# Performance work log

Measured on AMD Instinct MI355X. Metric: run time of the kernel, lower is better.

Reference implementation:

```python
import jax, jax.numpy as jnp
import numpy as np

HIDDEN = 2560
NUM_HEADS = 80
HEAD_DIM = 64
STATE = 128
N_GROUPS = 1
CONV_K = 4
CHUNK = 256
INTER = 2 * HIDDEN                       # 5120 = NUM_HEADS * HEAD_DIM
CONV_DIM = INTER + 2 * N_GROUPS * STATE  # 5376
PROJ = INTER + CONV_DIM + NUM_HEADS      # 10576
EPS = 1e-5
DT_MIN, DT_MAX = 0.0, 100.0


def segment_sum(x):
    # x: (..., T) -> (..., T, T); out[i, j] = sum_{j < k <= i} x[k], -inf above diag
    T = x.shape[-1]
    xe = jnp.broadcast_to(x[..., :, None], x.shape + (T,))  # [i, j] = x[i]
    mask_lo = jnp.tril(jnp.ones((T, T), dtype=bool), -1)
    seg = jnp.cumsum(jnp.where(mask_lo, xe, 0.0), axis=-2)
    mask = jnp.tril(jnp.ones((T, T), dtype=bool), 0)
    return jnp.where(mask, seg, -jnp.inf)


def setup_inputs() -> dict:
    key = jax.random.key(0)
    k0, k1, k2, k3 = jax.random.split(key, 4)
    x = jax.random.normal(k0, (2, 2048, HIDDEN), jnp.float32)
    in_proj_w = jax.random.normal(k1, (PROJ, HIDDEN), jnp.float32) * (HIDDEN ** -0.5)
    conv1d_w = jax.random.normal(k2, (CONV_DIM, CONV_K), jnp.float32) * (CONV_K ** -0.5)
    conv1d_b = jnp.zeros((CONV_DIM,), jnp.float32)
    A_log = jnp.log(jnp.arange(1, NUM_HEADS + 1, dtype=jnp.float32))
    D = jnp.ones((NUM_HEADS,), jnp.float32)
    dt_bias = jnp.ones((NUM_HEADS,), jnp.float32)
    norm_weight = jnp.ones((INTER,), jnp.float32)
    out_proj_w = jax.random.normal(k3, (HIDDEN, INTER), jnp.float32) * (INTER ** -0.5)
    return dict(input_states=x, in_proj_w=in_proj_w, conv1d_w=conv1d_w,
                conv1d_b=conv1d_b, A_log=A_log, D=D, dt_bias=dt_bias,
                norm_weight=norm_weight, out_proj_w=out_proj_w)


def _mamba2_forward(input_states, in_proj_w, conv1d_w, conv1d_b, A_log, D,
                    dt_bias, norm_weight, out_proj_w):
    b, s, _ = input_states.shape
    proj = input_states @ in_proj_w.T                       # (b, s, PROJ)
    gate, hs, dt = jnp.split(proj, [INTER, INTER + CONV_DIM], axis=-1)

    # causal depthwise conv1d + SiLU
    xT = jnp.transpose(hs, (0, 2, 1))                       # (b, conv_dim, s)
    xT = jnp.pad(xT, ((0, 0), (0, 0), (CONV_K - 1, 0)))
    conv = jax.lax.conv_general_dilated(
        xT, conv1d_w[:, None, :], (1,), 'VALID',
        feature_group_count=CONV_DIM, dimension_numbers=('NCH', 'OIH', 'NCH'))
    hs = jax.nn.silu(jnp.transpose(conv + conv1d_b[None, :, None], (0, 2, 1)))

    hs, B, C = jnp.split(hs, [INTER, INTER + N_GROUPS * STATE], axis=-1)
    A = -jnp.exp(A_log)                                     # (h,)
    dt = jnp.clip(jax.nn.softplus(dt + dt_bias), DT_MIN, DT_MAX)  # (b, s, h)

    X = hs.reshape(b, s, NUM_HEADS, HEAD_DIM)
    rep = NUM_HEADS // N_GROUPS
    B = jnp.repeat(B.reshape(b, s, N_GROUPS, STATE), rep, axis=2)
    C = jnp.repeat(C.reshape(b, s, N_GROUPS, STATE), rep, axis=2)

    pad = (-s) % CHUNK
    D_res = D[None, None, :, None] * jnp.pad(X, ((0, 0), (0, pad), (0, 0), (0, 0)))
    Xd = X * dt[..., None]                                  # discretized input
    dA = A[None, None, :] * dt                              # (b, s, h)

    def chunk(t):
        t = jnp.pad(t, [(0, 0), (0, pad)] + [(0, 0)] * (t.ndim - 2))
        return t.reshape(t.shape[0], -1, CHUNK, *t.shape[2:])

    Xc, Bc, Cc = chunk(Xd), chunk(B), chunk(C)              # (b, c, l, h, ...)
    Ac = jnp.transpose(chunk(dA), (0, 3, 1, 2))             # (b, h, c, l)
    A_cum = jnp.cumsum(Ac, axis=-1)

    # 1. intra-chunk (diagonal block) outputs
    L = jnp.exp(segment_sum(Ac))                            # (b, h, c, l, l)
    G = jnp.einsum('bclhn,bcshn->bhcls', Cc, Bc)
    Y_diag = jnp.einsum('bhcls,bcshp->bclhp', G * L, Xc)

    # 2. per-chunk final states
    decay_states = jnp.exp(A_cum[..., -1:] - A_cum)         # (b, h, c, l)
    states = jnp.einsum('bclhn,bhcl,bclhp->bchpn', Bc, decay_states, Xc)

    # 3. inter-chunk recurrence
    A_last = A_cum[..., -1]                                 # (b, h, c)
    decay_chunk = jnp.exp(segment_sum(jnp.pad(A_last, ((0, 0), (0, 0), (1, 0)))))
    states = jnp.concatenate([jnp.zeros_like(states[:, :1]), states], axis=1)
    new_states = jnp.einsum('bhzc,bchpn->bzhpn', decay_chunk, states)
    states = new_states[:, :-1]                             # (b, c, h, p, n)

    # 4. state -> output conversion
    Y_off = jnp.einsum('bclhn,bchpn,bhcl->bclhp', Cc, states, jnp.exp(A_cum))

    y = (Y_diag + Y_off).reshape(b, -1, NUM_HEADS, HEAD_DIM) + D_res
    y = y[:, :s].reshape(b, s, INTER)

    # gated RMSNorm
    y = y * jax.nn.silu(gate)
    var = jnp.mean(y * y, axis=-1, keepdims=True)
    y = y * jax.lax.rsqrt(var + EPS) * norm_weight
    return y @ out_proj_w.T


def reference(input_states, in_proj_w, conv1d_w, conv1d_b, A_log, D, dt_bias,
              norm_weight, out_proj_w):
    return _mamba2_forward(input_states, in_proj_w, conv1d_w, conv1d_b, A_log,
                           D, dt_bias, norm_weight, out_proj_w)
```

## Files before the change

kernel.cpp:

```cpp
#include <hip/hip_runtime.h>
#include <hip/hip_bf16.h>
#include <math.h>

#define HIDDEN   2560
#define NUM_HEADS 80
#define HEAD_DIM 64
#define STATE    128
#define CONV_K   4
#define CHUNK    256
#define INTER    (2*HIDDEN)
#define CONV_DIM (INTER + 2*STATE)
#define PROJ     (INTER + CONV_DIM + NUM_HEADS)
#define PROJ_PAD 10624
#define NBC      336
#define NBCP     384
#define EPS      1e-5f

#define BATCH 2
#define SEQ   2048
#define TOK   (BATCH*SEQ)
#define NC    (SEQ/CHUNK)
#define KSPL2 8
#define KCH2  (HIDDEN/KSPL2)

typedef __attribute__((ext_vector_type(8))) short bf16x8;
typedef __attribute__((ext_vector_type(4))) float f32x4;

#define MFMA16(a,b,c) __builtin_amdgcn_mfma_f32_16x16x32_bf16((a),(b),(c),0,0,0)

__device__ __forceinline__ unsigned short f2bf(float f){
    union{float f;unsigned u;}v; v.f=f;
    unsigned r = v.u + 0x7fffu + ((v.u>>16)&1u);
    return (unsigned short)(r>>16);
}
__device__ __forceinline__ float bf2f(unsigned short s){
    union{unsigned u;float f;}v; v.u = ((unsigned)s)<<16; return v.f;
}
__device__ __forceinline__ void unpack8(uint4 u, float* e){
    e[0]=bf2f((unsigned short)(u.x&0xffff)); e[1]=bf2f((unsigned short)(u.x>>16));
    e[2]=bf2f((unsigned short)(u.y&0xffff)); e[3]=bf2f((unsigned short)(u.y>>16));
    e[4]=bf2f((unsigned short)(u.z&0xffff)); e[5]=bf2f((unsigned short)(u.z>>16));
    e[6]=bf2f((unsigned short)(u.w&0xffff)); e[7]=bf2f((unsigned short)(u.w>>16));
}

__device__ __forceinline__ void gld16(const void* g, void* l){
    __builtin_amdgcn_global_load_lds((const __attribute__((address_space(1))) void*)g,
                                     (__attribute__((address_space(3))) void*)l, 16, 0, 0);
}

template<bool BF16OUT>
__global__ __launch_bounds__(256) void gemm_bf16(const unsigned short* __restrict__ A, int lda,
                                                 const unsigned short* __restrict__ B, int ldb,
                                                 void* __restrict__ Cv, int ldc, int K) {
    __shared__ unsigned short As[128][64];
    __shared__ unsigned short Bs[128][64];
    int tid = threadIdx.x;
    int lane = tid & 63, wid = tid >> 6;
    int wr = wid >> 1, wc = wid & 1;

    int bm, bn;
    if ((gridDim.y & 7) == 0) {
        int bid   = blockIdx.y * gridDim.x + blockIdx.x;
        int xcd   = bid & 7;
        int local = bid >> 3;
        int mrows = gridDim.y >> 3;
        bm = (xcd * mrows + (local % mrows)) * 128;
        bn = (local / mrows) * 128;
    } else {
        bm = blockIdx.y * 128;
        bn = blockIdx.x * 128;
    }

    f32x4 acc[4][4];
    #pragma unroll
    for (int i=0;i<4;i++)
        #pragma unroll
        for (int j=0;j<4;j++) acc[i][j] = (f32x4){0.f,0.f,0.f,0.f};

    int srow_off = lane >> 3;
    int sslot    = lane & 7;

    for (int k0 = 0; k0 < K; k0 += 64) {
        #pragma unroll
        for (int q=0;q<4;q++){
            int brow = (wid*4+q)*8;
            int row  = brow + srow_off;
            int sl   = sslot ^ (row & 7);
            gld16(A + (size_t)(bm + row)*lda + k0 + sl*8, &As[brow][0]);
            gld16(B + (size_t)(bn + row)*ldb + k0 + sl*8, &Bs[brow][0]);
        }
        __syncthreads();
        #pragma unroll
        for (int kk=0; kk<64; kk+=32){
            bf16x8 a[4], b[4];
            #pragma unroll
            for (int i=0;i<4;i++){
                int row = wr*64 + i*16 + (lane&15);
                int slot = ((kk>>3) + (lane>>4)) ^ (row & 7);
                a[i] = *(const bf16x8*)&As[row][slot*8];
            }
            #pragma unroll
            for (int j=0;j<4;j++){
                int row = wc*64 + j*16 + (lane&15);
                int slot = ((kk>>3) + (lane>>4)) ^ (row & 7);
                b[j] = *(const bf16x8*)&Bs[row][slot*8];
            }
            #pragma unroll
            for (int i=0;i<4;i++)
                #pragma unroll
                for (int j=0;j<4;j++)
                    acc[i][j] = MFMA16(a[i], b[j], acc[i][j]);
        }
        __syncthreads();
    }
    #pragma unroll
    for (int i=0;i<4;i++){
        int row0 = bm + wr*64 + i*16 + (lane>>4)*4;
        #pragma unroll
        for (int j=0;j<4;j++){
            int col = bn + wc*64 + j*16 + (lane&15);
            #pragma unroll
            for (int r=0;r<4;r++){
                if (BF16OUT)
                    ((unsigned short*)Cv)[(size_t)(row0+r)*ldc + col] = f2bf(acc[i][j][r]);
                else
                    ((float*)Cv)[(size_t)(row0+r)*ldc + col] = acc[i][j][r];
            }
        }
    }
}

__global__ __launch_bounds__(256) void bc_splitk_mfma(const unsigned short* __restrict__ xhi,
                                                      const unsigned short* __restrict__ xlo,
                                                      const unsigned short* __restrict__ whi,
                                                      const unsigned short* __restrict__ wlo,
                                                      float* __restrict__ Cpart) {
    __shared__ unsigned short As[128][64];
    __shared__ unsigned short Bs[128][64];
    int tid = threadIdx.x;
    int lane = tid & 63, wid = tid >> 6;
    int wr = wid >> 1, wc = wid & 1;
    int bn = blockIdx.x * 128, bm = blockIdx.y * 128, z = blockIdx.z;

    f32x4 acc[4][4];
    #pragma unroll
    for (int i=0;i<4;i++)
        #pragma unroll
        for (int j=0;j<4;j++) acc[i][j] = (f32x4){0.f,0.f,0.f,0.f};

    int srow_off = lane >> 3;
    int sslot    = lane & 7;

    for (int term = 0; term < 3; ++term){
        const unsigned short* A = (term==2) ? xlo : xhi;
        const unsigned short* B = (term==0) ? wlo : whi;
        for (int k0 = z*KCH2; k0 < z*KCH2 + KCH2; k0 += 64) {
            #pragma unroll
            for (int q=0;q<4;q++){
                int brow = (wid*4+q)*8;
                int row  = brow + srow_off;
                int sl   = sslot ^ (row & 7);
                gld16(A + (size_t)(bm + row)*HIDDEN + k0 + sl*8, &As[brow][0]);
                gld16(B + (size_t)(bn + row)*HIDDEN + k0 + sl*8, &Bs[brow][0]);
            }
            __syncthreads();
            #pragma unroll
            for (int kk=0; kk<64; kk+=32){
                bf16x8 a[4], b[4];
                #pragma unroll
                for (int i=0;i<4;i++){
                    int row = wr*64 + i*16 + (lane&15);
                    int slot = ((kk>>3) + (lane>>4)) ^ (row & 7);
                    a[i] = *(const bf16x8*)&As[row][slot*8];
                }
                #pragma unroll
                for (int j=0;j<4;j++){
                    int row = wc*64 + j*16 + (lane&15);
                    int slot = ((kk>>3) + (lane>>4)) ^ (row & 7);
                    b[j] = *(const bf16x8*)&Bs[row][slot*8];
                }
                #pragma unroll
                for (int i=0;i<4;i++)
                    #pragma unroll
                    for (int j=0;j<4;j++)
                        acc[i][j] = MFMA16(a[i], b[j], acc[i][j]);
            }
            __syncthreads();
        }
    }
    float* Cz = Cpart + (size_t)z*TOK*NBCP;
    #pragma unroll
    for (int i=0;i<4;i++){
        int row0 = bm + wr*64 + i*16 + (lane>>4)*4;
        #pragma unroll
        for (int j=0;j<4;j++){
            int col = bn + wc*64 + j*16 + (lane&15);
            #pragma unroll
            for (int r=0;r<4;r++)
                Cz[(size_t)(row0+r)*NBCP + col] = acc[i][j][r];
        }
    }
}

__global__ __launch_bounds__(256) void reduce_bc2(const float* __restrict__ part,
                                                  const float* __restrict__ dt_bias,
                                                  float* __restrict__ outBC,
                                                  float* __restrict__ dtbuf) {
    size_t i4 = (size_t)blockIdx.x*256 + threadIdx.x;
    if (i4 >= (size_t)TOK*NBCP/4) return;
    size_t i = i4*4;
    float4 s = *(const float4*)(part + i);
    #pragma unroll
    for (int z=1; z<KSPL2; z++){
        float4 v = *(const float4*)(part + (size_t)z*TOK*NBCP + i);
        s.x += v.x; s.y += v.y; s.z += v.z; s.w += v.w;
    }
    int col = (int)(i % NBCP);
    int t   = (int)(i / NBCP);
    if (col < 256) {
        *(float4*)(outBC + (size_t)t*NBC + col) = s;
    } else if (col < NBC) {
        int h = col - 256;
        float e[4] = {s.x, s.y, s.z, s.w};
        #pragma unroll
        for (int u=0;u<4;u++){
            float xv = e[u] + dt_bias[h+u];
            float sp = (xv > 20.f) ? xv : log1pf(expf(xv));
            e[u] = fminf(fmaxf(sp, 0.f), 100.f);
        }
        float4 o; o.x=e[0]; o.y=e[1]; o.z=e[2]; o.w=e[3];
        *(float4*)(dtbuf + (size_t)t*NUM_HEADS + h) = o;
    }
}

#define N4A ((size_t)TOK*HIDDEN/4)
#define N4B ((size_t)PROJ_PAD*HIDDEN/4)
#define N4C ((size_t)NBCP*HIDDEN/4)
__global__ __launch_bounds__(256) void prep_kernel(const float* __restrict__ x,
                                                   const float* __restrict__ in_w,
                                                   unsigned short* __restrict__ xhi,
                                                   unsigned short* __restrict__ xlo,
                                                   unsigned short* __restrict__ w1b,
                                                   unsigned short* __restrict__ wbc_hi,
                                                   unsigned short* __restrict__ wbc_lo) {
    size_t gid = (size_t)blockIdx.x*256 + threadIdx.x;
    if (gid < N4A) {
        size_t i = gid*4;
        float4 v = *(const float4*)(x + i);
        float e[4] = {v.x, v.y, v.z, v.w};
        ushort4 h, l;
        unsigned short* hp = (unsigned short*)&h;
        unsigned short* lp = (unsigned short*)&l;
        #pragma unroll
        for (int u=0;u<4;u++){
            unsigned short hv = f2bf(e[u]);
            hp[u] = hv;
            lp[u] = f2bf(e[u] - bf2f(hv));
        }
        *(ushort4*)(xhi + i) = h;
        *(ushort4*)(xlo + i) = l;
    } else if (gid < N4A + N4B) {
        size_t j = gid - N4A;
        size_t i = j*4;
        int row = (int)(i / HIDDEN);
        ushort4 o;
        if (row < PROJ){
            float4 v = *(const float4*)(in_w + i);
            o.x=f2bf(v.x); o.y=f2bf(v.y); o.z=f2bf(v.z); o.w=f2bf(v.w);
        } else { o.x=o.y=o.z=o.w=0; }
        *(ushort4*)(w1b + i) = o;
    } else {
        size_t j = gid - N4A - N4B;
        size_t i = j*4;
        int row = (int)(i / HIDDEN);
        int kk  = (int)(i % HIDDEN);
        ushort4 h, l;
        h.x=h.y=h.z=h.w=0; l.x=l.y=l.z=l.w=0;
        if (row < NBC){
            float4 v = *(const float4*)(in_w + (size_t)(2*INTER + row)*HIDDEN + kk);
            float e[4] = {v.x, v.y, v.z, v.w};
            unsigned short* hp = (unsigned short*)&h;
            unsigned short* lp = (unsigned short*)&l;
            #pragma unroll
            for (int u=0;u<4;u++){
                unsigned short hv = f2bf(e[u]);
                hp[u] = hv;
                lp[u] = f2bf(e[u] - bf2f(hv));
            }
        }
        *(ushort4*)(wbc_hi + i) = h;
        *(ushort4*)(wbc_lo + i) = l;
    }
}

__global__ __launch_bounds__(256) void cvt_bf16(const float* __restrict__ in,
                                                unsigned short* __restrict__ out, size_t n4){
    size_t i4 = (size_t)blockIdx.x*256 + threadIdx.x;
    if (i4 >= n4) return;
    size_t i = i4*4;
    float4 v = *(const float4*)(in+i);
    ushort4 o; o.x=f2bf(v.x); o.y=f2bf(v.y); o.z=f2bf(v.z); o.w=f2bf(v.w);
    *(ushort4*)(out+i) = o;
}

__global__ __launch_bounds__(256) void conv_fused(const unsigned short* __restrict__ projb,
                                                  const float* __restrict__ projBC,
                                                  const float* __restrict__ cw,
                                                  const float* __restrict__ cb,
                                                  unsigned short* __restrict__ XT,
                                                  float* __restrict__ xBC_BC,
                                                  unsigned short* __restrict__ BT) {
    __shared__ unsigned short raw[68][66];
    int bid = blockIdx.x;
    int tid = threadIdx.x;
    if (bid < (TOK/64)*(INTER/64)) {
        int bx = bid & 63, by = bid >> 6;
        int t0 = bx * 64, d0 = by * 64;
        int b  = t0 / SEQ;
        int s0 = t0 % SEQ;
        for (int f = tid; f < 67*8; f += 256){
            int r = f >> 3, g = f & 7;
            int sp = s0 - 3 + r;
            uint4 v;
            if (sp >= 0) v = *(const uint4*)(projb + ((size_t)(b*SEQ+sp))*PROJ_PAD + INTER + d0 + g*8);
            else { v.x=0u; v.y=0u; v.z=0u; v.w=0u; }
            unsigned int* dst = (unsigned int*)&raw[r][g*8];
            dst[0]=v.x; dst[1]=v.y; dst[2]=v.z; dst[3]=v.w;
        }
        __syncthreads();
        int t = tid & 63, dg = tid >> 6;
        #pragma unroll
        for (int dd = 0; dd < 16; dd++){
            int d = dg*16 + dd;
            float acc = cb[d0+d];
            #pragma unroll
            for (int j=0;j<CONV_K;j++)
                acc += cw[(d0+d)*CONV_K+j] * bf2f(raw[t+j][d]);
            float val = acc/(1.f+expf(-acc));
            XT[((size_t)(b*INTER + d0 + d))*SEQ + s0 + t] = f2bf(val);
        }
    } else {
        int idx = (bid - (TOK/64)*(INTER/64))*256 + tid;
        if (idx >= TOK*256) return;
        int d = idx & 255;
        int t = idx >> 8;
        int b = t / SEQ, sl = t % SEQ;
        int dc = INTER + d;
        float acc = cb[dc];
        #pragma unroll
        for (int j=0;j<CONV_K;j++){
            int sp = sl - (CONV_K-1) + j;
            if (sp >= 0)
                acc += cw[dc*CONV_K+j] * projBC[((size_t)(b*SEQ+sp))*NBC + d];
        }
        float val = acc / (1.f + expf(-acc));
        xBC_BC[(size_t)t*256 + d] = val;
        if (d < 128)
            BT[((size_t)(b*128 + d))*SEQ + sl] = f2bf(val);
    }
}

__global__ __launch_bounds__(256) void cumsum_kernel(const float* __restrict__ dtbuf,
                                                     const float* __restrict__ A_log,
                                                     float* __restrict__ A_cum) {
    int c = blockIdx.x, h = blockIdx.y, b = blockIdx.z;
    int l = threadIdx.x;
    float A = -expf(A_log[h]);
    float v = A * dtbuf[(size_t)(b*SEQ + c*CHUNK + l)*NUM_HEADS + h];
    __shared__ float buf[CHUNK];
    buf[l] = v;
    __syncthreads();
    for (int off=1; off<CHUNK; off<<=1){
        float t = (l>=off) ? buf[l-off] : 0.f;
        __syncthreads();
        buf[l] += t;
        __syncthreads();
    }
    A_cum[((size_t)b*NUM_HEADS + h)*SEQ + c*CHUNK + l] = buf[l];
}

__global__ __launch_bounds__(256) void g_kernel(const float* __restrict__ xBC_BC,
                                                unsigned short* __restrict__ G) {
    int p = blockIdx.x, c = blockIdx.y, b = blockIdx.z;
    int lt = 0, a0 = 0;
    while (a0 + lt + 1 <= p) { a0 += lt + 1; lt++; }
    int st = p - a0;
    int l0 = lt*64, s0 = st*64;
    __shared__ float Cs[64][68];
    __shared__ float Bs[64][68];
    int tid = threadIdx.x, ty = tid >> 4, tx = tid & 15;
    float acc[4][4];
    #pragma unroll
    for (int i=0;i<4;i++)
        #pragma unroll
        for (int j=0;j<4;j++) acc[i][j]=0.f;

    size_t rowC = ((size_t)(b*SEQ + c*CHUNK + l0))*256 + 128;
    size_t rowB = ((size_t)(b*SEQ + c*CHUNK + s0))*256;
    for (int kc=0; kc<2; kc++){
        #pragma unroll
        for (int it=0; it<4; it++){
            int f = tid + it*256;
            int r = f >> 4, c4 = f & 15;
            float4 cv = *(const float4*)(xBC_BC + rowC + (size_t)r*256 + kc*64 + c4*4);
            float4 bv = *(const float4*)(xBC_BC + rowB + (size_t)r*256 + kc*64 + c4*4);
            *(float4*)&Cs[r][c4*4] = cv;
            *(float4*)&Bs[r][c4*4] = bv;
        }
        __syncthreads();
        #pragma unroll 8
        for (int k=0;k<64;k++){
            float a[4], bb[4];
            #pragma unroll
            for (int i=0;i<4;i++) a[i] = Cs[ty*4+i][k];
            #pragma unroll
            for (int j=0;j<4;j++) bb[j] = Bs[tx*4+j][k];
            #pragma unroll
            for (int i=0;i<4;i++)
                #pragma unroll
                for (int j=0;j<4;j++) acc[i][j] += a[i]*bb[j];
        }
        __syncthreads();
    }
    size_t Gb = ((size_t)(b*NC + c)) << 16;
    #pragma unroll
    for (int i=0;i<4;i++){
        ushort4 g4;
        g4.x = f2bf(acc[i][0]); g4.y = f2bf(acc[i][1]);
        g4.z = f2bf(acc[i][2]); g4.w = f2bf(acc[i][3]);
        *(ushort4*)(G + Gb + (size_t)(l0 + ty*4 + i)*256 + s0 + tx*4) = g4;
    }
}

__global__ __launch_bounds__(256) void states_mfma(const unsigned short* __restrict__ XT,
                                                   const unsigned short* __restrict__ BT,
                                                   const float* __restrict__ dtbuf,
                                                   const float* __restrict__ A_cum,
                                                   float* __restrict__ statesT) {
    int c = blockIdx.x, h = blockIdx.y, b = blockIdx.z;
    __shared__ unsigned short Asx[64][64];
    __shared__ unsigned short Bsw[128][64];
    __shared__ float wl[CHUNK];
    int tid = threadIdx.x, lane = tid & 63, wid = tid >> 6;
    {
        const float* ac = A_cum + ((size_t)(b*NUM_HEADS+h))*SEQ + c*CHUNK;
        float Alast = ac[CHUNK-1];
        wl[tid] = expf(Alast - ac[tid]) * dtbuf[((size_t)(b*SEQ + c*CHUNK + tid))*NUM_HEADS + h];
    }
    __syncthreads();
    f32x4 acc[4][2];
    #pragma unroll
    for (int i=0;i<4;i++)
        #pragma unroll
        for (int j=0;j<2;j++) acc[i][j] = (f32x4){0.f,0.f,0.f,0.f};

    for (int kc = 0; kc < 4; kc++){
        int lbase = kc*64;
        #pragma unroll
        for (int q=0;q<2;q++){
            int brow = (wid*2+q)*8;
            int row  = brow + (lane>>3);
            int sl   = (lane&7) ^ (row & 7);
            gld16(XT + ((size_t)(b*INTER + h*HEAD_DIM + row))*SEQ + c*CHUNK + lbase + sl*8,
                  &Asx[brow][0]);
        }
        #pragma unroll
        for (int it=0; it<4; it++){
            int f = tid + it*256;
            int r = f >> 3, g = f & 7;
            uint4 v = *(const uint4*)(BT + ((size_t)(b*128 + r))*SEQ + c*CHUNK + lbase + g*8);
            float e[8]; unpack8(v, e);
            unsigned short o[8];
            #pragma unroll
            for (int u=0;u<8;u++) o[u] = f2bf(e[u] * wl[lbase + g*8 + u]);
            int slot = g ^ (r & 7);
            *(ushort4*)&Bsw[r][slot*8]   = *(ushort4*)&o[0];
            *(ushort4*)&Bsw[r][slot*8+4] = *(ushort4*)&o[4];
        }
        __syncthreads();
        #pragma unroll
        for (int kk=0; kk<64; kk+=32){
            bf16x8 a[4], bb[2];
            #pragma unroll
            for (int i=0;i<4;i++){
                int row = i*16 + (lane&15);
                int slot = ((kk>>3)+(lane>>4)) ^ (row&7);
                a[i] = *(const bf16x8*)&Asx[row][slot*8];
            }
            #pragma unroll
            for (int j=0;j<2;j++){
                int row = wid*32 + j*16 + (lane&15);
                int slot = ((kk>>3)+(lane>>4)) ^ (row&7);
                bb[j] = *(const bf16x8*)&Bsw[row][slot*8];
            }
            #pragma unroll
            for (int i=0;i<4;i++)
                #pragma unroll
                for (int j=0;j<2;j++)
                    acc[i][j] = MFMA16(a[i], bb[j], acc[i][j]);
        }
        __syncthreads();
    }
    size_t sb = ((size_t)((b*NC + c)*NUM_HEADS + h))*(HEAD_DIM*STATE);
    #pragma unroll
    for (int i=0;i<4;i++){
        #pragma unroll
        for (int j=0;j<2;j++){
            int n = wid*32 + j*16 + (lane&15);
            int p0 = i*16 + (lane>>4)*4;
            #pragma unroll
            for (int r=0;r<4;r++)
                statesT[sb + (size_t)(p0+r)*128 + n] = acc[i][j][r];
        }
    }
}

__global__ __launch_bounds__(256) void recur_kernel(const float* __restrict__ A_cum,
                                                    float* __restrict__ states) {
    int h = blockIdx.x, b = blockIdx.y;
    int tid = threadIdx.x;
    float Srun[32];
    #pragma unroll
    for (int i=0;i<32;i++) Srun[i]=0.f;
    const float* acum = A_cum + ((size_t)b*NUM_HEADS + h)*SEQ;
    for (int c=0;c<NC;c++){
        float alast = acum[c*CHUNK + CHUNK-1];
        float dec = expf(alast);
        size_t base = ((size_t)((b*NC + c)*NUM_HEADS + h))*(HEAD_DIM*STATE);
        #pragma unroll
        for (int i=0;i<32;i++){
            size_t idx = base + (size_t)tid + (size_t)i*256;
            float raw = states[idx];
            states[idx] = Srun[i];
            Srun[i] = Srun[i]*dec + raw;
        }
    }
}

__global__ __launch_bounds__(256) void yscan_mfma(const unsigned short* __restrict__ G,
                                                  const float* __restrict__ xBC_BC,
                                                  const unsigned short* __restrict__ XT,
                                                  const float* __restrict__ dtbuf,
                                                  const float* __restrict__ A_cum,
                                                  const float* __restrict__ statesT,
                                                  const float* __restrict__ Dvec,
                                                  unsigned short* __restrict__ projb) {
    int xb = blockIdx.x;
    int c = xb >> 2, lt = xb & 3;
    int h = blockIdx.y, b = blockIdx.z;
    int l0 = lt*64;
    __shared__ __align__(16) char pool[32768];
    unsigned short (*Cs)[128] = (unsigned short(*)[128])pool;
    unsigned short (*St)[128] = (unsigned short(*)[128])(pool + 16384);
    unsigned short (*Gw)[64]  = (unsigned short(*)[64])pool;
    unsigned short (*Xs)[64]  = (unsigned short(*)[64])(pool + 8192);
    float (*Ot)[68]           = (float(*)[68])pool;
    __shared__ float ac[CHUNK], dts[CHUNK];
    int tid = threadIdx.x, lane = tid & 63, wid = tid >> 6;
    ac[tid]  = A_cum[((size_t)(b*NUM_HEADS + h))*SEQ + c*CHUNK + tid];
    dts[tid] = dtbuf[((size_t)(b*SEQ + c*CHUNK + tid))*NUM_HEADS + h];
    __syncthreads();

    size_t stb = ((size_t)((b*NC + c)*NUM_HEADS + h))*(HEAD_DIM*STATE);
    #pragma unroll
    for (int it=0; it<8; it++){
        int f = tid + it*256;
        int r = f >> 5, c4 = f & 31;
        float4 v = *(const float4*)(xBC_BC + ((size_t)(b*SEQ + c*CHUNK + l0 + r))*256 + 128 + c4*4);
        unsigned short o[4] = {f2bf(v.x),f2bf(v.y),f2bf(v.z),f2bf(v.w)};
        int col = c4*4;
        int slot = (col>>3) ^ (r&7);
        *(ushort4*)&Cs[r][slot*8 + (col&7)] = *(ushort4*)o;
        float4 w = *(const float4*)(statesT + stb + (size_t)r*128 + c4*4);
        unsigned short o2[4] = {f2bf(w.x),f2bf(w.y),f2bf(w.z),f2bf(w.w)};
        *(ushort4*)&St[r][slot*8 + (col&7)] = *(ushort4*)o2;
    }
    __syncthreads();

    f32x4 acc1[4];
    #pragma unroll
    for (int j=0;j<4;j++) acc1[j] = (f32x4){0.f,0.f,0.f,0.f};
    #pragma unroll
    for (int kk=0; kk<128; kk+=32){
        int arow = wid*16 + (lane&15);
        int aslot = ((kk>>3)+(lane>>4)) ^ (arow&7);
        bf16x8 a = *(const bf16x8*)&Cs[arow][aslot*8];
        #pragma unroll
        for (int j=0;j<4;j++){
            int brow = j*16 + (lane&15);
            int bslot = ((kk>>3)+(lane>>4)) ^ (brow&7);
            bf16x8 bb = *(const bf16x8*)&St[brow][bslot*8];
            acc1[j] = MFMA16(a, bb, acc1[j]);
        }
    }
    float el[4];
    #pragma unroll
    for (int r=0;r<4;r++) el[r] = expf(ac[l0 + wid*16 + (lane>>4)*4 + r]);
    float master[4][4];
    #pragma unroll
    for (int j=0;j<4;j++)
        #pragma unroll
        for (int r=0;r<4;r++) master[j][r] = acc1[j][r]*el[r];
    __syncthreads();

    size_t Gb = ((size_t)(b*NC + c)) << 16;
    f32x4 acc2[4];
    #pragma unroll
    for (int j=0;j<4;j++) acc2[j] = (f32x4){0.f,0.f,0.f,0.f};
    for (int st=0; st<=lt; st++){
        int s0 = st*64;
        #pragma unroll
        for (int it=0; it<2; it++){
            int f = tid + it*256;
            int r = f >> 3, g = f & 7;
            uint4 v = *(const uint4*)(G + Gb + (size_t)(l0 + r)*256 + s0 + g*8);
            float e[8]; unpack8(v, e);
            float acl = ac[l0 + r];
            unsigned short o[8];
            #pragma unroll
            for (int u=0;u<8;u++){
                int s = s0 + g*8 + u;
                float w = (s <= l0 + r) ? expf(acl - ac[s])*dts[s] : 0.f;
                o[u] = f2bf(e[u]*w);
            }
            int slot = g ^ (r&7);
            *(ushort4*)&Gw[r][slot*8]   = *(ushort4*)&o[0];
            *(ushort4*)&Gw[r][slot*8+4] = *(ushort4*)&o[4];
        }
        #pragma unroll
        for (int q=0;q<2;q++){
            int brow = (wid*2+q)*8;
            int row  = brow + (lane>>3);
            int sl   = (lane&7) ^ (row&7);
            gld16(XT + ((size_t)(b*INTER + h*HEAD_DIM + row))*SEQ + c*CHUNK + s0 + sl*8,
                  &Xs[brow][0]);
        }
        __syncthreads();
        #pragma unroll
        for (int kk=0; kk<64; kk+=32){
            int arow = wid*16 + (lane&15);
            int aslot = ((kk>>3)+(lane>>4)) ^ (arow&7);
            bf16x8 a = *(const bf16x8*)&Gw[arow][aslot*8];
            #pragma unroll
            for (int j=0;j<4;j++){
                int brow = j*16 + (lane&15);
                int bslot = ((kk>>3)+(lane>>4)) ^ (brow&7);
                bf16x8 bb = *(const bf16x8*)&Xs[brow][bslot*8];
                acc2[j] = MFMA16(a, bb, acc2[j]);
            }
        }
        if (st < lt) __syncthreads();
    }

    float Dh = Dvec[h];
    #pragma unroll
    for (int j=0;j<4;j++){
        int p = j*16 + (lane&15);
        #pragma unroll
        for (int r=0;r<4;r++){
            int sl_ = wid*16 + (lane>>4)*4 + r;
            int slot = (sl_>>3) ^ (p&7);
            float xv = bf2f(Xs[p][slot*8 + (sl_&7)]);
            master[j][r] += acc2[j][r] + Dh*xv;
        }
    }
    __syncthreads();

    #pragma unroll
    for (int j=0;j<4;j++){
        int p = j*16 + (lane&15);
        #pragma unroll
        for (int r=0;r<4;r++)
            Ot[wid*16 + (lane>>4)*4 + r][p] = master[j][r];
    }
    __syncthreads();
    #pragma unroll
    for (int it=0; it<4; it++){
        int f = tid + it*256;
        int r = f >> 4, c4 = f & 15;
        ushort4 o;
        o.x = f2bf(Ot[r][c4*4+0]); o.y = f2bf(Ot[r][c4*4+1]);
        o.z = f2bf(Ot[r][c4*4+2]); o.w = f2bf(Ot[r][c4*4+3]);
        *(ushort4*)(projb + ((size_t)(b*SEQ + c*CHUNK + l0 + r))*PROJ_PAD + INTER + h*HEAD_DIM + c4*4) = o;
    }
}

__global__ __launch_bounds__(256) void gate_norm_kernel(const unsigned short* __restrict__ projb,
                                                        const float* __restrict__ normw,
                                                        unsigned short* __restrict__ yb) {
    int t = blockIdx.x;
    int tid = threadIdx.x;
    const unsigned short* row = projb + (size_t)t*PROJ_PAD;
    __shared__ float red[4];
    float vals[20];
    float ss = 0.f;
    #pragma unroll
    for (int i=0;i<5;i++){
        int j = (tid + i*256)*4;
        ushort4 g4 = *(const ushort4*)(row + j);
        ushort4 y4 = *(const ushort4*)(row + INTER + j);
        #pragma unroll
        for (int u=0;u<4;u++){
            float g = bf2f(((const unsigned short*)&g4)[u]);
            float y = bf2f(((const unsigned short*)&y4)[u]);
            float gv = g / (1.f + expf(-g));
            float v = y * gv;
            vals[i*4+u] = v;
            ss += v*v;
        }
    }
    #pragma unroll
    for (int off=32; off; off>>=1) ss += __shfl_xor(ss, off);
    if ((tid&63)==0) red[tid>>6] = ss;
    __syncthreads();
    float tot = red[0]+red[1]+red[2]+red[3];
    float inv = rsqrtf(tot/(float)INTER + EPS);
    #pragma unroll
    for (int i=0;i<5;i++){
        int j = (tid + i*256)*4;
        ushort4 o;
        o.x = f2bf(vals[i*4+0] * inv * normw[j+0]);
        o.y = f2bf(vals[i*4+1] * inv * normw[j+1]);
        o.z = f2bf(vals[i*4+2] * inv * normw[j+2]);
        o.w = f2bf(vals[i*4+3] * inv * normw[j+3]);
        *(ushort4*)(yb + (size_t)t*INTER + j) = o;
    }
}

extern "C" void kernel_launch(void* const* d_in, const int* in_sizes, int n_in,
                              void* d_out, int out_size, void* d_ws, size_t ws_size,
                              hipStream_t stream) {
    const float* x        = (const float*)d_in[0];
    const float* in_w     = (const float*)d_in[1];
    const float* conv_w   = (const float*)d_in[2];
    const float* conv_b   = (const float*)d_in[3];
    const float* A_log    = (const float*)d_in[4];
    const float* Dvec     = (const float*)d_in[5];
    const float* dt_bias  = (const float*)d_in[6];
    const float* norm_w   = (const float*)d_in[7];
    const float* out_w    = (const float*)d_in[8];
    float* out = (float*)d_out;
    (void)ws_size; (void)n_in; (void)in_sizes; (void)out_size;

    const size_t PROJB   = (size_t)TOK*PROJ_PAD*2;
    const size_t PROJBCB = (size_t)TOK*NBC*4;
    const size_t XTB     = (size_t)TOK*INTER*2;
    const size_t XBCBCB  = (size_t)TOK*256*4;
    const size_t BTB     = (size_t)BATCH*128*SEQ*2;
    const size_t GBYTES  = (size_t)BATCH*NC*CHUNK*CHUNK*2;
    const size_t DTB     = (size_t)TOK*NUM_HEADS*4;
    const size_t ACUMB   = DTB;
    const size_t STB     = (size_t)BATCH*NC*NUM_HEADS*HEAD_DIM*STATE*4;
    const size_t XHB   = (size_t)TOK*HIDDEN*2;
    const size_t WBCB  = (size_t)NBCP*HIDDEN*2;
    const size_t YBB   = (size_t)TOK*INTER*2;

    char* base = (char*)d_ws;
    size_t off = 0;
    unsigned short* projb  = (unsigned short*)(base + off); off += PROJB;
    float* projBC          = (float*)(base + off);          off += PROJBCB;
    unsigned short* XTp    = (unsigned short*)(base + off); off += XTB;
    float* xBC_BC          = (float*)(base + off);          off += XBCBCB;
    unsigned short* BTp    = (unsigned short*)(base + off); off += BTB;
    unsigned short* Gp     = (unsigned short*)(base + off); off += GBYTES;
    float* dtbuf           = (float*)(base + off);          off += DTB;
    float* A_cum           = (float*)(base + off);          off += ACUMB;
    float* statesT         = (float*)(base + off);          off += STB;
    char*  T               = base + off;
    unsigned short* xhi    = (unsigned short*)T;
    unsigned short* xlo    = (unsigned short*)(T + XHB);
    unsigned short* wbc_hi = (unsigned short*)(T + 2*XHB);
    unsigned short* wbc_lo = (unsigned short*)(T + 2*XHB + WBCB);
    unsigned short* w1b    = (unsigned short*)(T + 2*XHB + 2*WBCB);
    float* bcpart          = (float*)w1b;
    unsigned short* yb     = (unsigned short*)T;
    unsigned short* w2b    = (unsigned short*)(T + YBB);

    const size_t W2_E = (size_t)HIDDEN*INTER;

    {
        unsigned total_blocks = (unsigned)((N4A + N4B + N4C) / 256);
        prep_kernel<<<total_blocks, 256, 0, stream>>>(x, in_w, xhi, xlo, w1b, wbc_hi, wbc_lo);
    }
    gemm_bf16<true><<<dim3(PROJ_PAD/128, TOK/128), 256, 0, stream>>>(xhi, HIDDEN, w1b, HIDDEN,
                                                                     projb, PROJ_PAD, HIDDEN);
    bc_splitk_mfma<<<dim3(NBCP/128, TOK/128, KSPL2), 256, 0, stream>>>(xhi, xlo, wbc_hi, wbc_lo, bcpart);
    reduce_bc2<<<(unsigned)(((size_t)TOK*NBCP/4)/256), 256, 0, stream>>>(bcpart, dt_bias, projBC, dtbuf);
    conv_fused<<<(TOK/64)*(INTER/64) + TOK, 256, 0, stream>>>(projb, projBC, conv_w, conv_b,
                                                              XTp, xBC_BC, BTp);
    cvt_bf16<<<(unsigned)((W2_E/4+255)/256), 256, 0, stream>>>(out_w, w2b, W2_E/4);
    cumsum_kernel<<<dim3(NC, NUM_HEADS, BATCH), 256, 0, stream>>>(dtbuf, A_log, A_cum);
    g_kernel<<<dim3(10, NC, BATCH), 256, 0, stream>>>(xBC_BC, Gp);
    states_mfma<<<dim3(NC, NUM_HEADS, BATCH), 256, 0, stream>>>(XTp, BTp, dtbuf, A_cum, statesT);
    recur_kernel<<<dim3(NUM_HEADS, BATCH), 256, 0, stream>>>(A_cum, statesT);
    yscan_mfma<<<dim3(NC*4, NUM_HEADS, BATCH), 256, 0, stream>>>(Gp, xBC_BC, XTp, dtbuf, A_cum,
                                                                 statesT, Dvec, projb);
    gate_norm_kernel<<<TOK, 256, 0, stream>>>(projb, norm_w, yb);
    gemm_bf16<false><<<dim3(HIDDEN/128, TOK/128), 256, 0, stream>>>(yb, INTER, w2b, INTER,
                                                                    out, HIDDEN, INTER);
}
```

Measured before the change: 765.7 us.

## Trim in-proj GEMM padding, store chunk states in bf16, precompute bf16 C

The main input-projection GEMM now covers only 10240 output columns, the gate and x parts. The B, C and dt columns were already produced by the separate split-K path, so the padded tail is no longer computed. Inter-chunk states are stored and recurred in bf16 rather than fp32, which halves their traffic. The conv kernel also writes a bf16 copy of C so yscan can use direct global-to-LDS loads instead of converting fp32 per block. In states_mfma, the dt/decay weighting moves to the X operand and B is loaded directly. The risk is extra rounding error from keeping running states in bf16.

```diff
diff --git a/kernel.cpp b/kernel.cpp
--- a/kernel.cpp
+++ b/kernel.cpp
@@ -11,7 +11,7 @@
 #define INTER    (2*HIDDEN)
 #define CONV_DIM (INTER + 2*STATE)
 #define PROJ     (INTER + CONV_DIM + NUM_HEADS)
-#define PROJ_PAD 10624
+#define PROJ_PAD 10240
 #define NBC      336
 #define NBCP     384
 #define EPS      1e-5f
@@ -260,14 +260,10 @@
         *(ushort4*)(xhi + i) = h;
         *(ushort4*)(xlo + i) = l;
     } else if (gid < N4A + N4B) {
-        size_t j = gid - N4A;
-        size_t i = j*4;
-        int row = (int)(i / HIDDEN);
+        size_t i = (gid - N4A)*4;
+        float4 v = *(const float4*)(in_w + i);
         ushort4 o;
-        if (row < PROJ){
-            float4 v = *(const float4*)(in_w + i);
-            o.x=f2bf(v.x); o.y=f2bf(v.y); o.z=f2bf(v.z); o.w=f2bf(v.w);
-        } else { o.x=o.y=o.z=o.w=0; }
+        o.x=f2bf(v.x); o.y=f2bf(v.y); o.z=f2bf(v.z); o.w=f2bf(v.w);
         *(ushort4*)(w1b + i) = o;
     } else {
         size_t j = gid - N4A - N4B;
@@ -309,7 +305,8 @@
                                                   const float* __restrict__ cb,
                                                   unsigned short* __restrict__ XT,
                                                   float* __restrict__ xBC_BC,
-                                                  unsigned short* __restrict__ BT) {
+                                                  unsigned short* __restrict__ BT,
+                                                  unsigned short* __restrict__ Cb) {
     __shared__ unsigned short raw[68][66];
     int bid = blockIdx.x;
     int tid = threadIdx.x;
@@ -357,6 +354,8 @@
         xBC_BC[(size_t)t*256 + d] = val;
         if (d < 128)
             BT[((size_t)(b*128 + d))*SEQ + sl] = f2bf(val);
+        else
+            Cb[(size_t)t*128 + (d-128)] = f2bf(val);
     }
 }
 
@@ -436,10 +435,10 @@
                                                    const unsigned short* __restrict__ BT,
                                                    const float* __restrict__ dtbuf,
                                                    const float* __restrict__ A_cum,
-                                                   float* __restrict__ statesT) {
+                                                   unsigned short* __restrict__ statesT) {
     int c = blockIdx.x, h = blockIdx.y, b = blockIdx.z;
     __shared__ unsigned short Asx[64][64];
-    __shared__ unsigned short Bsw[128][64];
+    __shared__ unsigned short Bs[128][64];
     __shared__ float wl[CHUNK];
     int tid = threadIdx.x, lane = tid & 63, wid = tid >> 6;
     {
@@ -457,25 +456,24 @@
     for (int kc = 0; kc < 4; kc++){
         int lbase = kc*64;
         #pragma unroll
-        for (int q=0;q<2;q++){
-            int brow = (wid*2+q)*8;
+        for (int q=0;q<4;q++){
+            int brow = (wid*4+q)*8;
             int row  = brow + (lane>>3);
             int sl   = (lane&7) ^ (row & 7);
-            gld16(XT + ((size_t)(b*INTER + h*HEAD_DIM + row))*SEQ + c*CHUNK + lbase + sl*8,
-                  &Asx[brow][0]);
-        }
-        #pragma unroll
-        for (int it=0; it<4; it++){
+            gld16(BT + ((size_t)(b*128 + row))*SEQ + c*CHUNK + lbase + sl*8, &Bs[brow][0]);
+        }
+        #pragma unroll
+        for (int it=0; it<2; it++){
             int f = tid + it*256;
             int r = f >> 3, g = f & 7;
-            uint4 v = *(const uint4*)(BT + ((size_t)(b*128 + r))*SEQ + c*CHUNK + lbase + g*8);
+            uint4 v = *(const uint4*)(XT + ((size_t)(b*INTER + h*HEAD_DIM + r))*SEQ + c*CHUNK + lbase + g*8);
             float e[8]; unpack8(v, e);
             unsigned short o[8];
             #pragma unroll
             for (int u=0;u<8;u++) o[u] = f2bf(e[u] * wl[lbase + g*8 + u]);
             int slot = g ^ (r & 7);
-            *(ushort4*)&Bsw[r][slot*8]   = *(ushort4*)&o[0];
-            *(ushort4*)&Bsw[r][slot*8+4] = *(ushort4*)&o[4];
+            *(ushort4*)&Asx[r][slot*8]   = *(ushort4*)&o[0];
+            *(ushort4*)&Asx[r][slot*8+4] = *(ushort4*)&o[4];
         }
         __syncthreads();
         #pragma unroll
@@ -491,7 +489,7 @@
             for (int j=0;j<2;j++){
                 int row = wid*32 + j*16 + (lane&15);
                 int slot = ((kk>>3)+(lane>>4)) ^ (row&7);
-                bb[j] = *(const bf16x8*)&Bsw[row][slot*8];
+                bb[j] = *(const bf16x8*)&Bs[row][slot*8];
             }
             #pragma unroll
             for (int i=0;i<4;i++)
@@ -510,13 +508,13 @@
             int p0 = i*16 + (lane>>4)*4;
             #pragma unroll
             for (int r=0;r<4;r++)
-                statesT[sb + (size_t)(p0+r)*128 + n] = acc[i][j][r];
+                statesT[sb + (size_t)(p0+r)*128 + n] = f2bf(acc[i][j][r]);
         }
     }
 }
 
 __global__ __launch_bounds__(256) void recur_kernel(const float* __restrict__ A_cum,
-                                                    float* __restrict__ states) {
+                                                    unsigned short* __restrict__ states) {
     int h = blockIdx.x, b = blockIdx.y;
     int tid = threadIdx.x;
     float Srun[32];
@@ -530,19 +528,19 @@
         #pragma unroll
         for (int i=0;i<32;i++){
             size_t idx = base + (size_t)tid + (size_t)i*256;
-            float raw = states[idx];
-            states[idx] = Srun[i];
+            float raw = bf2f(states[idx]);
+            states[idx] = f2bf(Srun[i]);
             Srun[i] = Srun[i]*dec + raw;
         }
     }
 }
 
 __global__ __launch_bounds__(256) void yscan_mfma(const unsigned short* __restrict__ G,
-                                                  const float* __restrict__ xBC_BC,
+                                                  const unsigned short* __restrict__ Cb,
                                                   const unsigned short* __restrict__ XT,
                                                   const float* __restrict__ dtbuf,
                                                   const float* __restrict__ A_cum,
-                                                  const float* __restrict__ statesT,
+                                                  const unsigned short* __restrict__ statesT,
                                                   const float* __restrict__ Dvec,
                                                   unsigned short* __restrict__ projb) {
     int xb = blockIdx.x;
@@ -559,21 +557,15 @@
     int tid = threadIdx.x, lane = tid & 63, wid = tid >> 6;
     ac[tid]  = A_cum[((size_t)(b*NUM_HEADS + h))*SEQ + c*CHUNK + tid];
     dts[tid] = dtbuf[((size_t)(b*SEQ + c*CHUNK + tid))*NUM_HEADS + h];
-    __syncthreads();
 
     size_t stb = ((size_t)((b*NC + c)*NUM_HEADS + h))*(HEAD_DIM*STATE);
     #pragma unroll
-    for (int it=0; it<8; it++){
-        int f = tid + it*256;
-        int r = f >> 5, c4 = f & 31;
-        float4 v = *(const float4*)(xBC_BC + ((size_t)(b*SEQ + c*CHUNK + l0 + r))*256 + 128 + c4*4);
-        unsigned short o[4] = {f2bf(v.x),f2bf(v.y),f2bf(v.z),f2bf(v.w)};
-        int col = c4*4;
-        int slot = (col>>3) ^ (r&7);
-        *(ushort4*)&Cs[r][slot*8 + (col&7)] = *(ushort4*)o;
-        float4 w = *(const float4*)(statesT + stb + (size_t)r*128 + c4*4);
-        unsigned short o2[4] = {f2bf(w.x),f2bf(w.y),f2bf(w.z),f2bf(w.w)};
-        *(ushort4*)&St[r][slot*8 + (col&7)] = *(ushort4*)o2;
+    for (int q=0;q<4;q++){
+        int brow = (wid*4+q)*4;
+        int row  = brow + (lane>>4);
+        int sl   = (lane&15) ^ (row & 7);
+        gld16(Cb + ((size_t)(b*SEQ + c*CHUNK + l0 + row))*128 + sl*8, &Cs[brow][0]);
+        gld16(statesT + stb + (size_t)row*128 + sl*8, &St[brow][0]);
     }
     __syncthreads();
 
@@ -747,10 +739,11 @@
     const size_t XTB     = (size_t)TOK*INTER*2;
     const size_t XBCBCB  = (size_t)TOK*256*4;
     const size_t BTB     = (size_t)BATCH*128*SEQ*2;
+    const size_t CBB     = (size_t)TOK*128*2;
     const size_t GBYTES  = (size_t)BATCH*NC*CHUNK*CHUNK*2;
     const size_t DTB     = (size_t)TOK*NUM_HEADS*4;
     const size_t ACUMB   = DTB;
-    const size_t STB     = (size_t)BATCH*NC*NUM_HEADS*HEAD_DIM*STATE*4;
+    const size_t STB     = (size_t)BATCH*NC*NUM_HEADS*HEAD_DIM*STATE*2;
     const size_t XHB   = (size_t)TOK*HIDDEN*2;
     const size_t WBCB  = (size_t)NBCP*HIDDEN*2;
     const size_t YBB   = (size_t)TOK*INTER*2;
@@ -762,10 +755,11 @@
     unsigned short* XTp    = (unsigned short*)(base + off); off += XTB;
     float* xBC_BC          = (float*)(base + off);          off += XBCBCB;
     unsigned short* BTp    = (unsigned short*)(base + off); off += BTB;
+    unsigned short* Cbp    = (unsigned short*)(base + off); off += CBB;
     unsigned short* Gp     = (unsigned short*)(base + off); off += GBYTES;
     float* dtbuf           = (float*)(base + off);          off += DTB;
     float* A_cum           = (float*)(base + off);          off += ACUMB;
-    float* statesT         = (float*)(base + off);          off += STB;
+    unsigned short* statesT= (unsigned short*)(base + off); off += STB;
     char*  T               = base + off;
     unsigned short* xhi    = (unsigned short*)T;
     unsigned short* xlo    = (unsigned short*)(T + XHB);
@@ -787,13 +781,13 @@
     bc_splitk_mfma<<<dim3(NBCP/128, TOK/128, KSPL2), 256, 0, stream>>>(xhi, xlo, wbc_hi, wbc_lo, bcpart);
     reduce_bc2<<<(unsigned)(((size_t)TOK*NBCP/4)/256), 256, 0, stream>>>(bcpart, dt_bias, projBC, dtbuf);
     conv_fused<<<(TOK/64)*(INTER/64) + TOK, 256, 0, stream>>>(projb, projBC, conv_w, conv_b,
-                                                              XTp, xBC_BC, BTp);
+                                                              XTp, xBC_BC, BTp, Cbp);
     cvt_bf16<<<(unsigned)((W2_E/4+255)/256), 256, 0, stream>>>(out_w, w2b, W2_E/4);
     cumsum_kernel<<<dim3(NC, NUM_HEADS, BATCH), 256, 0, stream>>>(dtbuf, A_log, A_cum);
     g_kernel<<<dim3(10, NC, BATCH), 256, 0, stream>>>(xBC_BC, Gp);
     states_mfma<<<dim3(NC, NUM_HEADS, BATCH), 256, 0, stream>>>(XTp, BTp, dtbuf, A_cum, statesT);
     recur_kernel<<<dim3(NUM_HEADS, BATCH), 256, 0, stream>>>(A_cum, statesT);
-    yscan_mfma<<<dim3(NC*4, NUM_HEADS, BATCH), 256, 0, stream>>>(Gp, xBC_BC, XTp, dtbuf, A_cum,
+    yscan_mfma<<<dim3(NC*4, NUM_HEADS, BATCH), 256, 0, stream>>>(Gp, Cbp, XTp, dtbuf, A_cum,
                                                                  statesT, Dvec, projb);
     gate_norm_kernel<<<TOK, 256, 0, stream>>>(projb, norm_w, yb);
     gemm_bf16<false><<<dim3(HIDDEN/128, TOK/128), 256, 0, stream>>>(yb, INTER, w2b, INTER,
```

Result: faster. 726.8 us (-5.1%).
